# Kernel tuning notes

Measured on AMD Instinct MI355X. Metric: run time of the kernel, lower is better.

Reference implementation:

```python
import jax, jax.numpy as jnp
import numpy as np

N_NODES = 4096
JACOBI_ITERS = 10
EPS = 1e-5


def sym_laplacian_dense(edge_index, n):
    # L = I - D^{-1/2} A D^{-1/2}, duplicates in edge_index accumulate (as scipy COO does)
    row, col = edge_index[0], edge_index[1]
    A = jnp.zeros((n, n), jnp.float32).at[row, col].add(1.0)
    deg = A.sum(axis=1)
    dinv = jnp.where(deg > 0, 1.0 / jnp.sqrt(jnp.where(deg > 0, deg, 1.0)), 0.0)
    return jnp.eye(n, dtype=jnp.float32) - dinv[:, None] * A * dinv[None, :]


def jacobi_eig(a, iterations):
    # Faithful Jacobi: `iterations` Givens rotations, each zeroing the max |off-diag| entry.
    n = a.shape[0]
    upper = jnp.triu(jnp.ones((n, n), bool), k=1)

    def body(_, carry):
        a, p = carry
        idx = jnp.argmax(jnp.where(upper, jnp.abs(a), 0.0))
        k, l = idx // n, idx % n
        akl = a[k, l]
        aDiff = a[l, l] - a[k, k]
        akl_safe = jnp.where(akl == 0.0, 1.0, akl)
        aDiff_safe = jnp.where(aDiff == 0.0, 1.0, aDiff)
        phi = aDiff / (2.0 * akl_safe)
        t2 = 1.0 / (jnp.abs(phi) + jnp.sqrt(phi * phi + 1.0))
        t2 = jnp.where(phi < 0.0, -t2, t2)
        t1 = akl / aDiff_safe
        t = jnp.where(jnp.abs(akl) < jnp.abs(aDiff) * 1e-36, t1, t2)
        c = 1.0 / jnp.sqrt(t * t + 1.0)
        s = t * c
        # a <- G^T a G  (equivalent to the triangular in-place updates for symmetric a)
        ck, cl = a[:, k], a[:, l]
        a = a.at[:, k].set(c * ck - s * cl).at[:, l].set(s * ck + c * cl)
        rk, rl = a[k, :], a[l, :]
        a = a.at[k, :].set(c * rk - s * rl).at[l, :].set(s * rk + c * rl)
        a = a.at[k, l].set(0.0).at[l, k].set(0.0)
        pk, pl = p[:, k], p[:, l]
        p = p.at[:, k].set(c * pk - s * pl).at[:, l].set(s * pk + c * pl)
        return a, p

    a, p = jax.lax.fori_loop(0, iterations, body, (a, jnp.eye(n, dtype=a.dtype)))
    return jnp.diagonal(a), p


def setup_inputs() -> dict:
    key = jax.random.key(0)
    ks = jax.random.split(key, 8)
    n, cin, cout, r, e = N_NODES, 64, 64, 4, 100000
    x = jax.random.normal(ks[0], (n, cin), jnp.float32)
    src = jax.random.randint(ks[1], (e,), 0, n)
    dst = jax.random.randint(ks[2], (e,), 0, n)
    # symmetric graph (undirected), as the Jacobi solver assumes a symmetric Laplacian
    edge_index = jnp.stack([jnp.concatenate([src, dst]), jnp.concatenate([dst, src])]).astype(jnp.int64)
    stdv = 1.0 / np.sqrt(cin)
    real_weight = jax.random.uniform(ks[3], (cout, cin, r, 1), jnp.float32, -stdv, stdv)
    imag_weight = jax.random.uniform(ks[4], (cout, cin, r, 1), jnp.float32, -stdv, stdv)
    h = jax.random.uniform(ks[5], (cout, cin), jnp.float32, -stdv, stdv)
    c = jax.random.uniform(ks[6], (cout, cin, 1), jnp.float32, -stdv, stdv)
    bias = jnp.zeros((cout,), jnp.float32)
    return {"x": x, "edge_index": edge_index, "real_weight": real_weight,
            "imag_weight": imag_weight, "h": h, "c": c, "bias": bias}


def reference(x, edge_index, real_weight, imag_weight, h, c, bias):
    n = x.shape[0]
    r = real_weight.shape[2]
    L = sym_laplacian_dense(edge_index, n)
    w, U = jacobi_eig(L, JACOBI_ITERS)          # w: (N,), U: (N, N)
    aux = U.T @ x                                # (N, in)
    hw = h[:, :, None] * w[None, None, :]        # (out, in, N)
    a2 = jnp.where(hw > EPS,
                   2.0 * jnp.arctan(1.0 / jnp.where(hw > EPS, hw, 1.0)),
                   2.0)
    # theta[o,i,j,n] = a2[o,i,n] * (j+1)  -> (out, in, r, N)
    theta = a2[:, :, None, :] * jnp.arange(1, r + 1, dtype=x.dtype)[None, None, :, None]
    g = real_weight * jnp.cos(theta) - imag_weight * jnp.sin(theta)
    g = g.sum(axis=2) + c                        # (out, in, N)
    out = jnp.einsum('oin,ni->on', g, aux)       # Pmul + sum over in-channels
    output = U @ out.T + bias                    # (N, out); note: original's clamp(min=0) is a no-op
    return output
```

## Files before the change

kernel.cpp:

```cpp
#include <hip/hip_runtime.h>
#include <hip/hip_bf16.h>

#pragma clang fp contract(off)

#define N 4096
#define CIN 64
#define COUT 64
#define ITERS 10
#define MAXS 32
#define CANDMAX 384

typedef unsigned long long u64;

__device__ __forceinline__ u64 packkey(float v, unsigned j) {
    return ((u64)__float_as_uint(v) << 32) | (u64)(~j);
}
__device__ __forceinline__ u64 gkey(unsigned vb, unsigned row, unsigned col) {
    unsigned flat = (row << 12) | col;
    return ((u64)vb << 24) | (u64)((~flat) & 0xFFFFFFu);
}

__global__ void init_k(int* __restrict__ deg, int* __restrict__ fill) {
    int i = blockIdx.x * 256 + threadIdx.x;
    deg[i] = 0; fill[i] = 0;
}

__global__ void edges1_k(const int* __restrict__ ei, int* __restrict__ deg, int E) {
    int e = blockIdx.x * 256 + threadIdx.x;
    if (e < E) atomicAdd(&deg[ei[e]], 1);
}

__global__ void __launch_bounds__(1024) scan_k(const int* __restrict__ deg,
                                               int* __restrict__ rowptr,
                                               float* __restrict__ dinv) {
    __shared__ int ps[1024];
    int t = threadIdx.x, b = t * 4;
    int d0 = deg[b], d1 = deg[b + 1], d2 = deg[b + 2], d3 = deg[b + 3];
    int local = d0 + d1 + d2 + d3;
    ps[t] = local;
    __syncthreads();
    for (int off = 1; off < 1024; off <<= 1) {
        int v = (t >= off) ? ps[t - off] : 0;
        __syncthreads();
        ps[t] += v;
        __syncthreads();
    }
    int excl = ps[t] - local;
    rowptr[b] = excl; rowptr[b + 1] = excl + d0;
    rowptr[b + 2] = excl + d0 + d1; rowptr[b + 3] = excl + d0 + d1 + d2;
    if (t == 1023) rowptr[4096] = ps[1023];
    dinv[b]     = d0 > 0 ? 1.0f / sqrtf((float)d0) : 0.0f;
    dinv[b + 1] = d1 > 0 ? 1.0f / sqrtf((float)d1) : 0.0f;
    dinv[b + 2] = d2 > 0 ? 1.0f / sqrtf((float)d2) : 0.0f;
    dinv[b + 3] = d3 > 0 ? 1.0f / sqrtf((float)d3) : 0.0f;
}

__global__ void edges2_k(const int* __restrict__ ei, const int* __restrict__ rowptr,
                         int* __restrict__ fill, int* __restrict__ colidx, int E) {
    int e = blockIdx.x * 256 + threadIdx.x;
    if (e < E) {
        int r = ei[e], c = ei[E + e];
        int pos = rowptr[r] + atomicAdd(&fill[r], 1);
        colidx[pos] = c;
    }
}

__global__ void __launch_bounds__(64) rowmax0_k(
        const int* __restrict__ rowptr, const int* __restrict__ colidx,
        const float* __restrict__ dinv, const float* __restrict__ x,
        float* __restrict__ y, float* __restrict__ diag, u64* __restrict__ top24T,
        const float* __restrict__ hh, const float* __restrict__ cw,
        const float* __restrict__ rw, const float* __restrict__ iw,
        float2* __restrict__ hcT, float4* __restrict__ rwT, float4* __restrict__ iwT) {
    const int i = blockIdx.x, t = threadIdx.x;
    __shared__ float row[N];
    __shared__ u64 cand[CANDMAX];
    __shared__ int scnt;
    if (t < 3) {
        int ii = i >> 6, o = i & 63;
        int src = o * 64 + ii;
        if (t == 0) hcT[i] = make_float2(hh[src], cw[src]);
        else if (t == 1) rwT[i] = make_float4(rw[src * 4 + 0], rw[src * 4 + 1], rw[src * 4 + 2], rw[src * 4 + 3]);
        else iwT[i] = make_float4(iw[src * 4 + 0], iw[src * 4 + 1], iw[src * 4 + 2], iw[src * 4 + 3]);
    }
    int rs = rowptr[i], re = rowptr[i + 1];
    if (t == 0) { scnt = 0; row[i] = 0.0f; }
    __syncthreads();
    for (int e = rs + t; e < re; e += 64) { int c2 = colidx[e]; if (c2 >= i) row[c2] = 0.0f; }
    __syncthreads();
    for (int e = rs + t; e < re; e += 64) { int c2 = colidx[e]; if (c2 >= i) atomicAdd(&row[c2], 1.0f); }
    __syncthreads();
    float di = dinv[i];
    for (int e = rs + t; e < re; e += 64) {
        int c2 = colidx[e];
        if (c2 > i) {
            float v = -((di * row[c2]) * dinv[c2]);
            int idx = atomicAdd(&scnt, 1);
            if (idx < CANDMAX) cand[idx] = packkey(fabsf(v), (unsigned)c2);
        }
    }
    __syncthreads();
    int L = scnt < CANDMAX ? scnt : CANDMAX;
    for (int r = 0; r < 24; ++r) {
        u64 best = 0ull;
        for (int idx = t; idx < L; idx += 64) { u64 cc = cand[idx]; if (cc > best) best = cc; }
        for (int off = 32; off; off >>= 1) { u64 o = __shfl_xor(best, off, 64); if (o > best) best = o; }
        if (t == 0) top24T[(size_t)r * N + i] = best;
        for (int idx = t; idx < L; idx += 64) { if (cand[idx] == best) cand[idx] = 0ull; }
        __syncthreads();
    }
    if (t == 0) diag[i] = 1.0f - ((di * row[i]) * di);
    y[i * CIN + t] = x[i * CIN + t];
}

__global__ void __launch_bounds__(1024) jacobi_k(
        const int* __restrict__ rowptr, const int* __restrict__ colidx,
        const float* __restrict__ dinv,
        float* __restrict__ diag, const u64* __restrict__ top24T, float* __restrict__ y,
        float* __restrict__ rowS, float* __restrict__ colS,
        int* __restrict__ dslotG, int* __restrict__ slistG, int* __restrict__ nslotsG,
        int* __restrict__ rotk, int* __restrict__ rotl,
        float* __restrict__ rotc, float* __restrict__ rotsv) {
    __shared__ __align__(16) float cntK[N], cntL[N];
    __shared__ __align__(16) float rowKst[N], rowLst[N];
    __shared__ __align__(16) float dinvL[N];
    __shared__ u64 rmaxL[N];
    __shared__ float rvalL[N];
    __shared__ float diagL[N];
    __shared__ short dslotL[N];
    __shared__ u64 rmaxSlot[MAXS];
    __shared__ u64 w16[16], w16b[16];
    __shared__ float ovRowK[MAXS], ovRowL[MAXS], ovColK[MAXS], ovColL[MAXS];
    __shared__ int slistL[MAXS];
    __shared__ unsigned short sdirty[64];
    __shared__ int S_snd;
    const int t = threadIdx.x;

    u64 mb0 = 0ull;
    for (int i = t; i < N; i += 1024) {
        u64 kk = top24T[i];
        rmaxL[i] = kk;
        rvalL[i] = -__uint_as_float((unsigned)(kk >> 32));
        diagL[i] = diag[i];
        dinvL[i] = dinv[i];
        dslotL[i] = -1;
        unsigned col = (~(unsigned)kk) & 4095u;
        u64 gk = gkey((unsigned)(kk >> 32), (unsigned)i, col);
        if (gk > mb0) mb0 = gk;
    }
    for (int off = 32; off; off >>= 1) { u64 o = __shfl_down(mb0, off, 64); if (o > mb0) mb0 = o; }
    if ((t & 63) == 0) w16[t >> 6] = mb0;
    __syncthreads();
    u64 pivot = w16[0];
    for (int w = 1; w < 16; ++w) if (w16[w] > pivot) pivot = w16[w];
    int nsCur = 0;

    for (int it = 0; it < ITERS; ++it) {
        unsigned flat = (~(unsigned)pivot) & 0xFFFFFFu;
        const int k = (int)(flat >> 12), l = (int)(flat & 4095u);
        const float akl = rvalL[k];
        const float akk = diagL[k], all_ = diagL[l];
        float aDiff = all_ - akk;
        float akl_safe = (akl == 0.0f) ? 1.0f : akl;
        float aDiff_safe = (aDiff == 0.0f) ? 1.0f : aDiff;
        float phi = aDiff / (2.0f * akl_safe);
        float t2 = 1.0f / (fabsf(phi) + sqrtf(phi * phi + 1.0f));
        t2 = (phi < 0.0f) ? -t2 : t2;
        float t1 = akl / aDiff_safe;
        float tt = (fabsf(akl) < fabsf(aDiff) * 1e-36f) ? t1 : t2;
        const float c = 1.0f / sqrtf(tt * tt + 1.0f);
        const float s = tt * c;
        float a1kk = c * akk - s * akl;
        float a1kl = s * akk + c * akl;
        float a1lk = c * akl - s * all_;
        float a1ll = s * akl + c * all_;
        const float a2kk = c * a1kk - s * a1lk;
        const float a2ll = s * a1kl + c * a1ll;
        int ok = dslotL[k], ol = dslotL[l];
        const int nold = nsCur;
        const bool freshK = (ok < 0), freshL = (ol < 0);
        int sk2 = ok, sl3 = ol;
        { int ns = nsCur; if (freshK) sk2 = ns++; if (freshL) sl3 = ns++; nsCur = ns; }
        const int slotk = sk2, slotl = sl3;
        const float dk = dinvL[k], dl = dinvL[l];
        if (freshK) for (int j = t; j < N; j += 1024) cntK[j] = 0.0f;
        if (freshL) for (int j = t; j < N; j += 1024) cntL[j] = 0.0f;
        __syncthreads();
        if (t == 0) {
            rotk[it] = k; rotl[it] = l; rotc[it] = c; rotsv[it] = s;
            diagL[k] = a2kk; diagL[l] = a2ll;
            if (freshK) { slistL[slotk] = k; dslotL[k] = (short)slotk; }
            if (freshL) { slistL[slotl] = l; dslotL[l] = (short)slotl; }
            S_snd = 0;
        }
        if (t < CIN) {
            float yk = y[k * CIN + t], yl = y[l * CIN + t];
            y[k * CIN + t] = c * yk - s * yl;
            y[l * CIN + t] = s * yk + c * yl;
        }
        if (t >= 64 && t < 64 + nold) {
            int sl2 = t - 64;
            if (freshK) { ovRowK[sl2] = colS[(size_t)sl2 * N + k]; ovColK[sl2] = rowS[(size_t)sl2 * N + k]; }
            if (freshL) { ovRowL[sl2] = colS[(size_t)sl2 * N + l]; ovColL[sl2] = rowS[(size_t)sl2 * N + l]; }
        }
        if (freshK) for (int e = rowptr[k] + t; e < rowptr[k + 1]; e += 1024) atomicAdd(&cntK[colidx[e]], 1.0f);
        if (freshL) for (int e = rowptr[l] + t; e < rowptr[l + 1]; e += 1024) atomicAdd(&cntL[colidx[e]], 1.0f);
        __syncthreads();
        u64 bk = packkey(0.0f, 4095u), bl = packkey(0.0f, 4095u);
        {
            const int j0 = t * 4;
            float4 dj4 = *reinterpret_cast<const float4*>(dinvL + j0);
            float4 bK4, bL4, cK4, cL4;
            if (freshK) {
                float4 cnt = *reinterpret_cast<const float4*>(cntK + j0);
#pragma unroll
                for (int m = 0; m < 4; ++m) {
                    float cn = (&cnt.x)[m], dj = (&dj4.x)[m];
                    (&bK4.x)[m] = -((dk * cn) * dj);
                    (&cK4.x)[m] = -((dj * cn) * dk);
                }
            } else {
                bK4 = *reinterpret_cast<const float4*>(rowS + (size_t)ok * N + j0);
                cK4 = *reinterpret_cast<const float4*>(colS + (size_t)ok * N + j0);
            }
            if (freshL) {
                float4 cnt = *reinterpret_cast<const float4*>(cntL + j0);
#pragma unroll
                for (int m = 0; m < 4; ++m) {
                    float cn = (&cnt.x)[m], dj = (&dj4.x)[m];
                    (&bL4.x)[m] = -((dl * cn) * dj);
                    (&cL4.x)[m] = -((dj * cn) * dl);
                }
            } else {
                bL4 = *reinterpret_cast<const float4*>(rowS + (size_t)ol * N + j0);
                cL4 = *reinterpret_cast<const float4*>(colS + (size_t)ol * N + j0);
            }
            float4 nrK4, nrL4, ncK4, ncL4;
#pragma unroll
            for (int m = 0; m < 4; ++m) {
                int j = j0 + m;
                float bK = (&bK4.x)[m], bL = (&bL4.x)[m];
                float cK = (&cK4.x)[m], cL = (&cL4.x)[m];
                float nrk, nrl, nck, ncl;
                if (j == k)      { nrk = a2kk; nrl = 0.0f; nck = a2kk; ncl = 0.0f; }
                else if (j == l) { nrk = 0.0f; nrl = a2ll; nck = 0.0f; ncl = a2ll; }
                else {
                    int sl2 = dslotL[j];
                    if (sl2 >= 0 && sl2 < nold) {
                        if (freshK) { bK = ovRowK[sl2]; cK = ovColK[sl2]; }
                        if (freshL) { bL = ovRowL[sl2]; cL = ovColL[sl2]; }
                    }
                    nrk = c * bK - s * bL; nrl = s * bK + c * bL;
                    nck = c * cK - s * cL; ncl = s * cK + c * cL;
                }
                (&nrK4.x)[m] = nrk; (&nrL4.x)[m] = nrl;
                (&ncK4.x)[m] = nck; (&ncL4.x)[m] = ncl;
                if (j > k) { u64 kk = packkey(fabsf(nrk), (unsigned)j); if (kk > bk) bk = kk; }
                if (j > l) { u64 kk = packkey(fabsf(nrl), (unsigned)j); if (kk > bl) bl = kk; }
            }
            *reinterpret_cast<float4*>(rowS + (size_t)slotk * N + j0) = nrK4;
            *reinterpret_cast<float4*>(rowS + (size_t)slotl * N + j0) = nrL4;
            *reinterpret_cast<float4*>(colS + (size_t)slotk * N + j0) = ncK4;
            *reinterpret_cast<float4*>(colS + (size_t)slotl * N + j0) = ncL4;
            *reinterpret_cast<float4*>(rowKst + j0) = nrK4;
            *reinterpret_cast<float4*>(rowLst + j0) = nrL4;
            *reinterpret_cast<float4*>(cntK + j0) = ncK4;
            *reinterpret_cast<float4*>(cntL + j0) = ncL4;
        }
        for (int off = 32; off; off >>= 1) {
            u64 o = __shfl_down(bk, off, 64); if (o > bk) bk = o;
            u64 o2 = __shfl_down(bl, off, 64); if (o2 > bl) bl = o2;
        }
        if ((t & 63) == 0) { w16[t >> 6] = bk; w16b[t >> 6] = bl; }
        __syncthreads();
        if (t == 0) {
            u64 b1 = w16[0], b2 = w16b[0];
            for (int w = 1; w < 16; ++w) { if (w16[w] > b1) b1 = w16[w]; if (w16b[w] > b2) b2 = w16b[w]; }
            unsigned j1 = (~(unsigned)b1) & 4095u, j2 = (~(unsigned)b2) & 4095u;
            rvalL[k] = rowKst[j1];
            rvalL[l] = rowLst[j2];
            rmaxSlot[slotk] = gkey((unsigned)(b1 >> 32), (unsigned)k, j1);
            rmaxSlot[slotl] = gkey((unsigned)(b2 >> 32), (unsigned)l, j2);
        }
        if (t >= 64 && t < 64 + nold) {
            int sl2 = t - 64;
            int js = slistL[sl2];
            if (js != k && js != l) {
                float vkj = rowKst[js];
                float vlj = rowLst[js];
                float vjk = cntK[js];
                float vjl = cntL[js];
                colS[(size_t)sl2 * N + k] = vkj;
                colS[(size_t)sl2 * N + l] = vlj;
                rowS[(size_t)sl2 * N + k] = vjk;
                rowS[(size_t)sl2 * N + l] = vjl;
                u64 cached = rmaxSlot[sl2];
                unsigned cj = ((~(unsigned)cached) & 0xFFFFFFu) & 4095u;
                bool kc = (k > js), lc = (l > js);
                u64 ck2 = kc ? gkey(__float_as_uint(fabsf(vjk)), (unsigned)js, (unsigned)k) : 0ull;
                u64 cl2 = lc ? gkey(__float_as_uint(fabsf(vjl)), (unsigned)js, (unsigned)l) : 0ull;
                bool stale = false; u64 base = cached; bool useOld = true;
                if (kc && cj == (unsigned)k)      { if (ck2 < cached) stale = true; else { base = 0ull; useOld = false; } }
                else if (lc && cj == (unsigned)l) { if (cl2 < cached) stale = true; else { base = 0ull; useOld = false; } }
                if (!stale) {
                    if (kc || lc) {
                        u64 mm = base; float mv = useOld ? rvalL[js] : 0.0f;
                        if (ck2 > mm) { mm = ck2; mv = vjk; }
                        if (cl2 > mm) { mm = cl2; mv = vjl; }
                        rmaxSlot[sl2] = mm; rvalL[js] = mv;
                    }
                } else { int d2 = atomicAdd(&S_snd, 1); sdirty[d2] = (unsigned short)sl2; }
            }
        }
        u64 myBest = 0ull;
#pragma unroll
        for (int m = 0; m < 4; ++m) {
            int j = t + 1024 * m;
            if (dslotL[j] >= 0) continue;
            float nck = cntK[j], ncl = cntL[j];
            u64 cached = rmaxL[j];
            unsigned cj = (~(unsigned)cached) & 4095u;
            bool kc = (k > j), lc = (l > j);
            u64 ck2 = kc ? packkey(fabsf(nck), (unsigned)k) : 0ull;
            u64 cl2 = lc ? packkey(fabsf(ncl), (unsigned)l) : 0ull;
            bool stale = false; u64 base = cached; bool useOld = true;
            if (kc && cj == (unsigned)k)      { if (ck2 < cached) stale = true; else { base = 0ull; useOld = false; } }
            else if (lc && cj == (unsigned)l) { if (cl2 < cached) stale = true; else { base = 0ull; useOld = false; } }
            if (!stale) {
                if (kc || lc) {
                    u64 mm = base; float mv = useOld ? rvalL[j] : 0.0f;
                    if (ck2 > mm) { mm = ck2; mv = nck; }
                    if (cl2 > mm) { mm = cl2; mv = ncl; }
                    rmaxL[j] = mm; rvalL[j] = mv;
                }
            } else {
                u64 bKey = 0ull; float bVal = 0.0f;
                for (int cc = 0; cc < 24; ++cc) {
                    u64 cand = top24T[(size_t)cc * N + j];
                    unsigned col = (~(unsigned)cand) & 4095u;
                    if (dslotL[col] < 0) {
                        bKey = cand;
                        bVal = -__uint_as_float((unsigned)(cand >> 32));
                        break;
                    }
                }
                for (int sl = 0; sl < nsCur; ++sl) {
                    if (sl == slotk || sl == slotl) continue;
                    int js = slistL[sl];
                    if (js > j) {
                        float v = colS[(size_t)sl * N + j];
                        u64 kk2 = packkey(fabsf(v), (unsigned)js);
                        if (kk2 > bKey) { bKey = kk2; bVal = v; }
                    }
                }
                if (kc && ck2 > bKey) { bKey = ck2; bVal = nck; }
                if (lc && cl2 > bKey) { bKey = cl2; bVal = ncl; }
                rmaxL[j] = bKey; rvalL[j] = bVal;
            }
            u64 fin = rmaxL[j];
            u64 gk = gkey((unsigned)(fin >> 32), (unsigned)j, (~(unsigned)fin) & 4095u);
            if (gk > myBest) myBest = gk;
        }
        __syncthreads();
        const int nd = S_snd;
        for (int d = 0; d < nd; ++d) {
            int sl2 = sdirty[d];
            int ir = slistL[sl2];
            u64 bb = packkey(0.0f, 4095u);
            int jb = t * 4;
            float4 v4 = *reinterpret_cast<const float4*>(rowS + (size_t)sl2 * N + jb);
#pragma unroll
            for (int m = 0; m < 4; ++m) {
                int j = jb + m;
                if (j > ir) {
                    u64 kk = packkey(fabsf((&v4.x)[m]), (unsigned)j);
                    if (kk > bb) bb = kk;
                }
            }
            for (int off = 32; off; off >>= 1) { u64 o = __shfl_down(bb, off, 64); if (o > bb) bb = o; }
            if ((t & 63) == 0) w16[t >> 6] = bb;
            __syncthreads();
            if (t == 0) {
                u64 b = w16[0];
                for (int w = 1; w < 16; ++w) if (w16[w] > b) b = w16[w];
                unsigned js2 = (~(unsigned)b) & 4095u;
                rmaxSlot[sl2] = gkey((unsigned)(b >> 32), (unsigned)ir, js2);
                rvalL[ir] = rowS[(size_t)sl2 * N + js2];
            }
            __syncthreads();
        }
        if (t < nsCur) { u64 o2 = rmaxSlot[t]; if (o2 > myBest) myBest = o2; }
        for (int off = 32; off; off >>= 1) { u64 o = __shfl_down(myBest, off, 64); if (o > myBest) myBest = o; }
        if ((t & 63) == 0) w16[t >> 6] = myBest;
        __syncthreads();
        pivot = w16[0];
        for (int w = 1; w < 16; ++w) if (w16[w] > pivot) pivot = w16[w];
    }
    for (int i = t; i < N; i += 1024) {
        diag[i] = diagL[i];
        dslotG[i] = (int)dslotL[i];
    }
    if (t < nsCur) slistG[t] = slistL[t];
    if (t == 0) *nslotsG = nsCur;
}

__global__ void __launch_bounds__(1024) spectral_store_k(
        const float* __restrict__ diag, const float* __restrict__ y,
        const float2* __restrict__ hcT, const float4* __restrict__ rwT,
        const float4* __restrict__ iwT, const float* __restrict__ bias,
        const int* __restrict__ dslot, const int* __restrict__ slistG,
        const int* __restrict__ nslotsG,
        const int* __restrict__ rotk, const int* __restrict__ rotl,
        const float* __restrict__ rotc, const float* __restrict__ rotsv,
        float* __restrict__ out) {
    __shared__ float saux[16][CIN];
    __shared__ float zloc[MAXS][COUT];
    const int t = threadIdx.x;
    const float C2 = -0.41614683654714241f;
    const float S2 = 0.90929742682568170f;
    if (blockIdx.x < 256) {
        int o = t & 63, nl = t >> 6;
        int n = blockIdx.x * 16 + nl;
        saux[nl][o] = y[n * CIN + o];
        __syncthreads();
        float wn = diag[n];
        float acc = 0.0f;
        for (int i = 0; i < CIN; ++i) {
            float2 hc = hcT[i * 64 + o];
            float hw = hc.x * wn;
            float t2v = hw * hw;
            float inv = 1.0f / (t2v + 1.0f);
            float c1 = (t2v - 1.0f) * inv;
            float s1 = (2.0f * hw) * inv;
            if (!(hw > 1e-5f)) { c1 = C2; s1 = S2; }
            float4 rwv = rwT[i * 64 + o];
            float4 iwv = iwT[i * 64 + o];
            float g = hc.y;
            float cj = c1, sj = s1;
            g += rwv.x * cj - iwv.x * sj;
            float cn = cj * c1 - sj * s1; float sn = sj * c1 + cj * s1; cj = cn; sj = sn;
            g += rwv.y * cj - iwv.y * sj;
            cn = cj * c1 - sj * s1; sn = sj * c1 + cj * s1; cj = cn; sj = sn;
            g += rwv.z * cj - iwv.z * sj;
            cn = cj * c1 - sj * s1; sn = sj * c1 + cj * s1; cj = cn; sj = sn;
            g += rwv.w * cj - iwv.w * sj;
            acc += g * saux[nl][i];
        }
        if (dslot[n] < 0) out[n * COUT + o] = acc + bias[o];
    } else {
        int ns = *nslotsG;
        int o = t & 63, d = t >> 6;
        for (int dd = d; dd < ns; dd += 16) {
            int r = slistG[dd];
            float wn = diag[r];
            float acc = 0.0f;
            for (int i = 0; i < CIN; ++i) {
                float2 hc = hcT[i * 64 + o];
                float hw = hc.x * wn;
                float t2v = hw * hw;
                float inv = 1.0f / (t2v + 1.0f);
                float c1 = (t2v - 1.0f) * inv;
                float s1 = (2.0f * hw) * inv;
                if (!(hw > 1e-5f)) { c1 = C2; s1 = S2; }
                float4 rwv = rwT[i * 64 + o];
                float4 iwv = iwT[i * 64 + o];
                float g = hc.y;
                float cj = c1, sj = s1;
                g += rwv.x * cj - iwv.x * sj;
                float cn = cj * c1 - sj * s1; float sn = sj * c1 + cj * s1; cj = cn; sj = sn;
                g += rwv.y * cj - iwv.y * sj;
                cn = cj * c1 - sj * s1; sn = sj * c1 + cj * s1; cj = cn; sj = sn;
                g += rwv.z * cj - iwv.z * sj;
                cn = cj * c1 - sj * s1; sn = sj * c1 + cj * s1; cj = cn; sj = sn;
                g += rwv.w * cj - iwv.w * sj;
                acc += g * y[r * CIN + i];
            }
            zloc[dd][o] = acc;
        }
        __syncthreads();
        if (t < 64) {
            for (int i = ITERS - 1; i >= 0; --i) {
                int k = rotk[i], l = rotl[i];
                float c = rotc[i], s = rotsv[i];
                int sk = dslot[k], sl = dslot[l];
                float zk = zloc[sk][t], zl = zloc[sl][t];
                zloc[sk][t] = c * zk + s * zl;
                zloc[sl][t] = -s * zk + c * zl;
            }
        }
        __syncthreads();
        for (int dd = d; dd < ns; dd += 16) {
            out[slistG[dd] * COUT + o] = zloc[dd][o] + bias[o];
        }
    }
}

extern "C" void kernel_launch(void* const* d_in, const int* in_sizes, int n_in,
                              void* d_out, int out_size, void* d_ws, size_t ws_size,
                              hipStream_t stream) {
    const float* x   = (const float*)d_in[0];
    const int*   ei  = (const int*)d_in[1];
    const float* rw  = (const float*)d_in[2];
    const float* iw  = (const float*)d_in[3];
    const float* hh  = (const float*)d_in[4];
    const float* cw  = (const float*)d_in[5];
    const float* bias= (const float*)d_in[6];
    float* out = (float*)d_out;

    float* rowS = (float*)d_ws;
    float* colS = rowS + (size_t)MAXS * N;
    float* y    = colS + (size_t)MAXS * N;
    float2* hcT = (float2*)(y + N * CIN);
    float4* rwT = (float4*)(hcT + 4096);
    float4* iwT = rwT + 4096;
    float* dinv = (float*)(iwT + 4096);
    float* diag = dinv + N;
    u64* top24T = (u64*)(diag + N);
    int* rowptr = (int*)(top24T + 24 * (size_t)N);
    int* fill   = rowptr + 4100;
    int* deg    = fill + N;
    int* slist  = deg + N;
    int* nslots = slist + 64;
    int* dslot  = nslots + 4;
    int* rotk   = dslot + N;
    int* rotl   = rotk + 16;
    float* rotc = (float*)(rotl + 16);
    float* rotsv= rotc + 16;
    int* colidx = (int*)(rotsv + 16);

    int E = in_sizes[1] / 2;
    int eb = (E + 255) / 256;

    init_k<<<16, 256, 0, stream>>>(deg, fill);
    edges1_k<<<eb, 256, 0, stream>>>(ei, deg, E);
    scan_k<<<1, 1024, 0, stream>>>(deg, rowptr, dinv);
    edges2_k<<<eb, 256, 0, stream>>>(ei, rowptr, fill, colidx, E);
    rowmax0_k<<<N, 64, 0, stream>>>(rowptr, colidx, dinv, x, y, diag, top24T,
                                    hh, cw, rw, iw, hcT, rwT, iwT);

    jacobi_k<<<1, 1024, 0, stream>>>(rowptr, colidx, dinv, diag, top24T,
                                     y, rowS, colS, dslot, slist, nslots,
                                     rotk, rotl, rotc, rotsv);

    spectral_store_k<<<257, 1024, 0, stream>>>(diag, y, hcT, rwT, iwT, bias,
                                               dslot, slist, nslots,
                                               rotk, rotl, rotc, rotsv, out);
}
```

Measured before the change: 292.6 us.

## Split spectral stage into uniform compute kernel and separate rotation/store kernel

The weight transposition moves out of the per-row rowmax kernel into the init kernel as extra blocks. The spectral kernel that had one special block recomputing touched rows serially is split in two. A uniform spectral_k writes z for all nodes to a workspace buffer, and store_fused_k applies the inverse Givens rotations in global memory and writes the output. This removes the serialized tail block but adds a kernel launch and a global round trip of z.

```diff
diff --git a/kernel.cpp b/kernel.cpp
--- a/kernel.cpp
+++ b/kernel.cpp
@@ -20,9 +20,23 @@
     return ((u64)vb << 24) | (u64)((~flat) & 0xFFFFFFu);
 }
 
-__global__ void init_k(int* __restrict__ deg, int* __restrict__ fill) {
-    int i = blockIdx.x * 256 + threadIdx.x;
-    deg[i] = 0; fill[i] = 0;
+__global__ void init_prep_k(int* __restrict__ deg, int* __restrict__ fill,
+                            const float* __restrict__ hh, const float* __restrict__ cw,
+                            const float* __restrict__ rw, const float* __restrict__ iw,
+                            float2* __restrict__ hcT, float4* __restrict__ rwT,
+                            float4* __restrict__ iwT) {
+    int b = blockIdx.x;
+    if (b < 16) {
+        int i = b * 256 + threadIdx.x;
+        deg[i] = 0; fill[i] = 0;
+    } else {
+        int idx = (b - 16) * 256 + threadIdx.x;
+        int i = idx >> 6, o = idx & 63;
+        int src = o * 64 + i;
+        hcT[idx] = make_float2(hh[src], cw[src]);
+        rwT[idx] = make_float4(rw[src * 4 + 0], rw[src * 4 + 1], rw[src * 4 + 2], rw[src * 4 + 3]);
+        iwT[idx] = make_float4(iw[src * 4 + 0], iw[src * 4 + 1], iw[src * 4 + 2], iw[src * 4 + 3]);
+    }
 }
 
 __global__ void edges1_k(const int* __restrict__ ei, int* __restrict__ deg, int E) {
@@ -68,21 +82,11 @@
 __global__ void __launch_bounds__(64) rowmax0_k(
         const int* __restrict__ rowptr, const int* __restrict__ colidx,
         const float* __restrict__ dinv, const float* __restrict__ x,
-        float* __restrict__ y, float* __restrict__ diag, u64* __restrict__ top24T,
-        const float* __restrict__ hh, const float* __restrict__ cw,
-        const float* __restrict__ rw, const float* __restrict__ iw,
-        float2* __restrict__ hcT, float4* __restrict__ rwT, float4* __restrict__ iwT) {
+        float* __restrict__ y, float* __restrict__ diag, u64* __restrict__ top24T) {
     const int i = blockIdx.x, t = threadIdx.x;
     __shared__ float row[N];
     __shared__ u64 cand[CANDMAX];
     __shared__ int scnt;
-    if (t < 3) {
-        int ii = i >> 6, o = i & 63;
-        int src = o * 64 + ii;
-        if (t == 0) hcT[i] = make_float2(hh[src], cw[src]);
-        else if (t == 1) rwT[i] = make_float4(rw[src * 4 + 0], rw[src * 4 + 1], rw[src * 4 + 2], rw[src * 4 + 3]);
-        else iwT[i] = make_float4(iw[src * 4 + 0], iw[src * 4 + 1], iw[src * 4 + 2], iw[src * 4 + 3]);
-    }
     int rs = rowptr[i], re = rowptr[i + 1];
     if (t == 0) { scnt = 0; row[i] = 0.0f; }
     __syncthreads();
@@ -404,93 +408,69 @@
     if (t == 0) *nslotsG = nsCur;
 }
 
-__global__ void __launch_bounds__(1024) spectral_store_k(
+__global__ void __launch_bounds__(1024) spectral_k(
         const float* __restrict__ diag, const float* __restrict__ y,
         const float2* __restrict__ hcT, const float4* __restrict__ rwT,
-        const float4* __restrict__ iwT, const float* __restrict__ bias,
+        const float4* __restrict__ iwT, float* __restrict__ z) {
+    int o = threadIdx.x & 63;
+    int nl = threadIdx.x >> 6;
+    int n = blockIdx.x * 16 + nl;
+    __shared__ float saux[16][CIN];
+    saux[nl][o] = y[n * CIN + o];
+    __syncthreads();
+    float wn = diag[n];
+    const float C2 = -0.41614683654714241f;
+    const float S2 = 0.90929742682568170f;
+    float acc = 0.0f;
+    for (int i = 0; i < CIN; ++i) {
+        float2 hc = hcT[i * 64 + o];
+        float hw = hc.x * wn;
+        float t2v = hw * hw;
+        float inv = 1.0f / (t2v + 1.0f);
+        float c1 = (t2v - 1.0f) * inv;
+        float s1 = (2.0f * hw) * inv;
+        if (!(hw > 1e-5f)) { c1 = C2; s1 = S2; }
+        float4 rwv = rwT[i * 64 + o];
+        float4 iwv = iwT[i * 64 + o];
+        float g = hc.y;
+        float cj = c1, sj = s1;
+        g += rwv.x * cj - iwv.x * sj;
+        float cn = cj * c1 - sj * s1; float sn = sj * c1 + cj * s1; cj = cn; sj = sn;
+        g += rwv.y * cj - iwv.y * sj;
+        cn = cj * c1 - sj * s1; sn = sj * c1 + cj * s1; cj = cn; sj = sn;
+        g += rwv.z * cj - iwv.z * sj;
+        cn = cj * c1 - sj * s1; sn = sj * c1 + cj * s1; cj = cn; sj = sn;
+        g += rwv.w * cj - iwv.w * sj;
+        acc += g * saux[nl][i];
+    }
+    z[(size_t)n * COUT + o] = acc;
+}
+
+__global__ void store_fused_k(
+        float* __restrict__ z, const float* __restrict__ bias,
         const int* __restrict__ dslot, const int* __restrict__ slistG,
         const int* __restrict__ nslotsG,
         const int* __restrict__ rotk, const int* __restrict__ rotl,
         const float* __restrict__ rotc, const float* __restrict__ rotsv,
         float* __restrict__ out) {
-    __shared__ float saux[16][CIN];
-    __shared__ float zloc[MAXS][COUT];
-    const int t = threadIdx.x;
-    const float C2 = -0.41614683654714241f;
-    const float S2 = 0.90929742682568170f;
-    if (blockIdx.x < 256) {
-        int o = t & 63, nl = t >> 6;
-        int n = blockIdx.x * 16 + nl;
-        saux[nl][o] = y[n * CIN + o];
-        __syncthreads();
-        float wn = diag[n];
-        float acc = 0.0f;
-        for (int i = 0; i < CIN; ++i) {
-            float2 hc = hcT[i * 64 + o];
-            float hw = hc.x * wn;
-            float t2v = hw * hw;
-            float inv = 1.0f / (t2v + 1.0f);
-            float c1 = (t2v - 1.0f) * inv;
-            float s1 = (2.0f * hw) * inv;
-            if (!(hw > 1e-5f)) { c1 = C2; s1 = S2; }
-            float4 rwv = rwT[i * 64 + o];
-            float4 iwv = iwT[i * 64 + o];
-            float g = hc.y;
-            float cj = c1, sj = s1;
-            g += rwv.x * cj - iwv.x * sj;
-            float cn = cj * c1 - sj * s1; float sn = sj * c1 + cj * s1; cj = cn; sj = sn;
-            g += rwv.y * cj - iwv.y * sj;
-            cn = cj * c1 - sj * s1; sn = sj * c1 + cj * s1; cj = cn; sj = sn;
-            g += rwv.z * cj - iwv.z * sj;
-            cn = cj * c1 - sj * s1; sn = sj * c1 + cj * s1; cj = cn; sj = sn;
-            g += rwv.w * cj - iwv.w * sj;
-            acc += g * saux[nl][i];
-        }
-        if (dslot[n] < 0) out[n * COUT + o] = acc + bias[o];
-    } else {
+    int t = threadIdx.x;
+    if (blockIdx.x < 1024) {
+        int idx = blockIdx.x * 256 + t;
+        int row = idx >> 6;
+        if (dslot[row] < 0) out[idx] = z[idx] + bias[idx & 63];
+    } else if (t < 64) {
+        for (int i = ITERS - 1; i >= 0; --i) {
+            int k = rotk[i], l = rotl[i];
+            float c = rotc[i], s = rotsv[i];
+            float zk = z[k * COUT + t];
+            float zl = z[l * COUT + t];
+            z[k * COUT + t] = c * zk + s * zl;
+            z[l * COUT + t] = -s * zk + c * zl;
+        }
         int ns = *nslotsG;
-        int o = t & 63, d = t >> 6;
-        for (int dd = d; dd < ns; dd += 16) {
-            int r = slistG[dd];
-            float wn = diag[r];
-            float acc = 0.0f;
-            for (int i = 0; i < CIN; ++i) {
-                float2 hc = hcT[i * 64 + o];
-                float hw = hc.x * wn;
-                float t2v = hw * hw;
-                float inv = 1.0f / (t2v + 1.0f);
-                float c1 = (t2v - 1.0f) * inv;
-                float s1 = (2.0f * hw) * inv;
-                if (!(hw > 1e-5f)) { c1 = C2; s1 = S2; }
-                float4 rwv = rwT[i * 64 + o];
-                float4 iwv = iwT[i * 64 + o];
-                float g = hc.y;
-                float cj = c1, sj = s1;
-                g += rwv.x * cj - iwv.x * sj;
-                float cn = cj * c1 - sj * s1; float sn = sj * c1 + cj * s1; cj = cn; sj = sn;
-                g += rwv.y * cj - iwv.y * sj;
-                cn = cj * c1 - sj * s1; sn = sj * c1 + cj * s1; cj = cn; sj = sn;
-                g += rwv.z * cj - iwv.z * sj;
-                cn = cj * c1 - sj * s1; sn = sj * c1 + cj * s1; cj = cn; sj = sn;
-                g += rwv.w * cj - iwv.w * sj;
-                acc += g * y[r * CIN + i];
-            }
-            zloc[dd][o] = acc;
-        }
-        __syncthreads();
-        if (t < 64) {
-            for (int i = ITERS - 1; i >= 0; --i) {
-                int k = rotk[i], l = rotl[i];
-                float c = rotc[i], s = rotsv[i];
-                int sk = dslot[k], sl = dslot[l];
-                float zk = zloc[sk][t], zl = zloc[sl][t];
-                zloc[sk][t] = c * zk + s * zl;
-                zloc[sl][t] = -s * zk + c * zl;
-            }
-        }
-        __syncthreads();
-        for (int dd = d; dd < ns; dd += 16) {
-            out[slistG[dd] * COUT + o] = zloc[dd][o] + bias[o];
+        for (int d = 0; d < ns; ++d) {
+            int r = slistG[d];
+            out[r * COUT + t] = z[r * COUT + t] + bias[t];
         }
     }
 }
@@ -510,7 +490,8 @@
     float* rowS = (float*)d_ws;
     float* colS = rowS + (size_t)MAXS * N;
     float* y    = colS + (size_t)MAXS * N;
-    float2* hcT = (float2*)(y + N * CIN);
+    float* z    = y + N * CIN;
+    float2* hcT = (float2*)(z + N * COUT);
     float4* rwT = (float4*)(hcT + 4096);
     float4* iwT = rwT + 4096;
     float* dinv = (float*)(iwT + 4096);
@@ -531,18 +512,17 @@
     int E = in_sizes[1] / 2;
     int eb = (E + 255) / 256;
 
-    init_k<<<16, 256, 0, stream>>>(deg, fill);
+    init_prep_k<<<32, 256, 0, stream>>>(deg, fill, hh, cw, rw, iw, hcT, rwT, iwT);
     edges1_k<<<eb, 256, 0, stream>>>(ei, deg, E);
     scan_k<<<1, 1024, 0, stream>>>(deg, rowptr, dinv);
     edges2_k<<<eb, 256, 0, stream>>>(ei, rowptr, fill, colidx, E);
-    rowmax0_k<<<N, 64, 0, stream>>>(rowptr, colidx, dinv, x, y, diag, top24T,
-                                    hh, cw, rw, iw, hcT, rwT, iwT);
+    rowmax0_k<<<N, 64, 0, stream>>>(rowptr, colidx, dinv, x, y, diag, top24T);
 
     jacobi_k<<<1, 1024, 0, stream>>>(rowptr, colidx, dinv, diag, top24T,
                                      y, rowS, colS, dslot, slist, nslots,
                                      rotk, rotl, rotc, rotsv);
 
-    spectral_store_k<<<257, 1024, 0, stream>>>(diag, y, hcT, rwT, iwT, bias,
-                                               dslot, slist, nslots,
-                                               rotk, rotl, rotc, rotsv, out);
-}
+    spectral_k<<<N / 16, 1024, 0, stream>>>(diag, y, hcT, rwT, iwT, z);
+    store_fused_k<<<1025, 256, 0, stream>>>(z, bias, dslot, slist, nslots,
+                                            rotk, rotl, rotc, rotsv, out);
+}
```

New measurement: 267.1 us. 8.7% less time.
